# Performance work log

Measured on AMD Instinct MI355X. Metric: run time of the kernel, lower is better.

The kernel has to match this reference:

```python
import jax, jax.numpy as jnp
import numpy as np

B, CN, CC, D, V = 65536, 16, 16, 128, 65
EPS = 1e-05

def setup_inputs() -> dict:
    key = jax.random.key(0)
    ks = jax.random.split(key, 7)
    x_num = jax.random.normal(ks[0], (B, CN), dtype=jnp.float32)
    x_cat = jax.random.randint(ks[1], (B, CC), 0, V, dtype=jnp.int32)
    means = jax.random.normal(ks[2], (CN,), dtype=jnp.float32)
    stds = jax.random.uniform(ks[3], (CN,), dtype=jnp.float32, minval=0.5, maxval=2.0)
    lin_W = jax.random.normal(ks[4], (CN, D), dtype=jnp.float32) * 0.02  # Linear(1,D) weight per numeric attr
    lin_b = jax.random.normal(ks[5], (CN, D), dtype=jnp.float32) * 0.02
    emb = jax.random.normal(ks[6], (CC, V, D), dtype=jnp.float32) * 0.02  # stacked embedding tables
    return {"x_num": x_num, "means": means, "stds": stds, "lin_W": lin_W,
            "lin_b": lin_b, "emb": emb, "x_cat": x_cat}

def reference(x_num, means, stds, lin_W, lin_b, emb, x_cat):
    # numeric attrs: sigmoid((x - mean)/(std + eps)) -> Linear(1,D), summed over attrs
    z = jax.nn.sigmoid((x_num - means) / (stds + EPS))          # [B, CN]
    h = jnp.einsum('bi,id->bd', z, lin_W) + lin_b.sum(axis=0)   # [B, D]
    # categorical attrs: per-attr embedding lookup, summed over attrs
    gathered = emb[jnp.arange(emb.shape[0]), x_cat]             # [B, CC, D]
    return h + gathered.sum(axis=1)                              # [B, D]
```

## Files before the change

kernel.cpp:

```cpp
#include <hip/hip_runtime.h>


constexpr int CN = 16;
constexpr int CC = 16;
constexpr int D  = 128;
constexpr int V  = 65;
constexpr float EPS = 1e-5f;

constexpr int W      = 16;
constexpr int NSLICE = D / W;
constexpr int RPB    = 512;
constexpr int TILE   = 64;
constexpr int NTILE  = RPB / TILE;
constexpr int PAD    = 20;

__device__ __forceinline__ unsigned short f2bf(float f) {
    unsigned u = __float_as_uint(f);
    u = (u + 0x7fffu + ((u >> 16) & 1u)) >> 16;
    return (unsigned short)u;
}

__device__ __forceinline__ void fma4(float s, const float4& w, float4& a) {
    a.x += s * w.x; a.y += s * w.y; a.z += s * w.z; a.w += s * w.w;
}

__device__ __forceinline__ void gacc(const unsigned short* p, float4& a) {
    const uint2 g = *(const uint2*)p;
    a.x += __uint_as_float(g.x << 16);
    a.y += __uint_as_float(g.x & 0xffff0000u);
    a.z += __uint_as_float(g.y << 16);
    a.w += __uint_as_float(g.y & 0xffff0000u);
}

__global__ __launch_bounds__(256, 3) void embed_att_kernel(
    const float* __restrict__ x_num,
    const float* __restrict__ means,
    const float* __restrict__ stds,
    const float* __restrict__ lin_W,
    const float* __restrict__ lin_b,
    const float* __restrict__ emb,
    const int*  __restrict__ x_cat,
    float* __restrict__ out)
{
    __shared__ unsigned short emb_s[CC * V * W];
    __shared__ float z_s[2][TILE][PAD];
    __shared__ int   idx_s[2][TILE][PAD];

    const int tid = threadIdx.x;
    const int l   = tid & 3;
    const int l4  = l * 4;
    const int rr  = tid >> 2;
    const int d0  = blockIdx.y * W;
    const int row_base = blockIdx.x * RPB;

    float4 wf[CN];
    float4 bs = make_float4(0.f, 0.f, 0.f, 0.f);
#pragma unroll
    for (int i = 0; i < CN; ++i) {
        wf[i] = *(const float4*)&lin_W[i * D + d0 + l4];
        const float4 b = *(const float4*)&lin_b[i * D + d0 + l4];
        bs.x += b.x; bs.y += b.y; bs.z += b.z; bs.w += b.w;
    }
    const float4 mm = *(const float4*)&means[l4];
    const float4 sv = *(const float4*)&stds[l4];
    const float LOG2E = 1.44269504088896340736f;
    float4 inv;
    inv.x = -LOG2E / (sv.x + EPS); inv.y = -LOG2E / (sv.y + EPS);
    inv.z = -LOG2E / (sv.z + EPS); inv.w = -LOG2E / (sv.w + EPS);

    for (int j = tid; j < CC * V * W / 4; j += 256) {
        const int seg = j >> 2, k = j & 3;
        const float4 e = *(const float4*)&emb[seg * D + d0 + k * 4];
        uint2 p;
        p.x = (unsigned)f2bf(e.x) | ((unsigned)f2bf(e.y) << 16);
        p.y = (unsigned)f2bf(e.z) | ((unsigned)f2bf(e.w) << 16);
        *(uint2*)&emb_s[seg * W + k * 4] = p;
    }

    float4 xf; int4 xi;
    {
        const int row = row_base + rr;
        xf = *(const float4*)&x_num[row * CN + l4];
        xi = *(const int4*)&x_cat[row * CC + l4];
    }

    for (int t = 0; t < NTILE; ++t) {
        const int buf = t & 1;
        float4 z;
        z.x = 1.f / (1.f + __builtin_amdgcn_exp2f((xf.x - mm.x) * inv.x));
        z.y = 1.f / (1.f + __builtin_amdgcn_exp2f((xf.y - mm.y) * inv.y));
        z.z = 1.f / (1.f + __builtin_amdgcn_exp2f((xf.z - mm.z) * inv.z));
        z.w = 1.f / (1.f + __builtin_amdgcn_exp2f((xf.w - mm.w) * inv.w));
        *(float4*)&z_s[buf][rr][l4] = z;
        *(int4*)&idx_s[buf][rr][l4] = xi;
        __syncthreads();

        if (t + 1 < NTILE) {
            const int row = row_base + (t + 1) * TILE + rr;
            xf = *(const float4*)&x_num[row * CN + l4];
            xi = *(const int4*)&x_cat[row * CC + l4];
        }

        const int4 i0 = *(const int4*)&idx_s[buf][rr][0];
        const int4 i1 = *(const int4*)&idx_s[buf][rr][4];
        const int4 i2 = *(const int4*)&idx_s[buf][rr][8];
        const int4 i3 = *(const int4*)&idx_s[buf][rr][12];
        const float4 z0 = *(const float4*)&z_s[buf][rr][0];
        const float4 z1 = *(const float4*)&z_s[buf][rr][4];
        const float4 z2 = *(const float4*)&z_s[buf][rr][8];
        const float4 z3 = *(const float4*)&z_s[buf][rr][12];

        float4 acc = bs;
        fma4(z0.x, wf[0],  acc); fma4(z0.y, wf[1],  acc);
        fma4(z0.z, wf[2],  acc); fma4(z0.w, wf[3],  acc);
        fma4(z1.x, wf[4],  acc); fma4(z1.y, wf[5],  acc);
        fma4(z1.z, wf[6],  acc); fma4(z1.w, wf[7],  acc);
        fma4(z2.x, wf[8],  acc); fma4(z2.y, wf[9],  acc);
        fma4(z2.z, wf[10], acc); fma4(z2.w, wf[11], acc);
        fma4(z3.x, wf[12], acc); fma4(z3.y, wf[13], acc);
        fma4(z3.z, wf[14], acc); fma4(z3.w, wf[15], acc);

#define GAT(c, ix) gacc(&emb_s[((c) * V + (ix)) * W + l4], acc)
        GAT(0,  i0.x); GAT(1,  i0.y); GAT(2,  i0.z); GAT(3,  i0.w);
        GAT(4,  i1.x); GAT(5,  i1.y); GAT(6,  i1.z); GAT(7,  i1.w);
        GAT(8,  i2.x); GAT(9,  i2.y); GAT(10, i2.z); GAT(11, i2.w);
        GAT(12, i3.x); GAT(13, i3.y); GAT(14, i3.z); GAT(15, i3.w);
#undef GAT

        const int row = row_base + t * TILE + rr;
        *(float4*)&out[row * D + d0 + l4] = acc;
    }
}

extern "C" void kernel_launch(void* const* d_in, const int* in_sizes, int n_in,
                              void* d_out, int out_size, void* d_ws, size_t ws_size,
                              hipStream_t stream) {
    const float* x_num = (const float*)d_in[0];
    const float* means = (const float*)d_in[1];
    const float* stds  = (const float*)d_in[2];
    const float* lin_W = (const float*)d_in[3];
    const float* lin_b = (const float*)d_in[4];
    const float* emb   = (const float*)d_in[5];
    const int*   x_cat = (const int*)d_in[6];
    float* out = (float*)d_out;

    const int B      = in_sizes[0] / CN;
    const int nchunk = B / RPB;

    dim3 grid(nchunk, NSLICE, 1);
    embed_att_kernel<<<grid, 256, 0, stream>>>(x_num, means, stds, lin_W, lin_b,
                                               emb, x_cat, out);
}
```

Measured before the change: 99.45 us.

## Make z/idx staging wave-private, drop per-tile barrier, pad embedding rows

Each wavefront now stages its own 16 rows of sigmoid values and indices in a private shared-memory slice, so the per-tile block-wide barrier is removed and only one barrier remains after the embedding table load. The bf16 embedding rows in LDS are padded from 16 to 20 elements to spread random gather accesses across banks. The aim is to cut barrier stalls and LDS bank conflicts. The cost is more LDS for the table (about 41.6 KB versus 33 KB), which may limit blocks per CU, and the code relies on the wavefront lockstep ordering of each wave's own write and subsequent read.

```diff
diff --git a/kernel.cpp b/kernel.cpp
--- a/kernel.cpp
+++ b/kernel.cpp
@@ -12,7 +12,8 @@
 constexpr int RPB    = 512;
 constexpr int TILE   = 64;
 constexpr int NTILE  = RPB / TILE;
-constexpr int PAD    = 20;
+constexpr int EPAD   = 20;
+constexpr int ZPAD   = 20;
 
 __device__ __forceinline__ unsigned short f2bf(float f) {
     unsigned u = __float_as_uint(f);
@@ -42,14 +43,16 @@
     const int*  __restrict__ x_cat,
     float* __restrict__ out)
 {
-    __shared__ unsigned short emb_s[CC * V * W];
-    __shared__ float z_s[2][TILE][PAD];
-    __shared__ int   idx_s[2][TILE][PAD];
+    __shared__ unsigned short emb_s[CC * V * EPAD];
+    __shared__ float z_s[4][16][ZPAD];
+    __shared__ int   idx_s[4][16][ZPAD];
 
     const int tid = threadIdx.x;
     const int l   = tid & 3;
     const int l4  = l * 4;
     const int rr  = tid >> 2;
+    const int w   = tid >> 6;
+    const int rw  = rr & 15;
     const int d0  = blockIdx.y * W;
     const int row_base = blockIdx.x * RPB;
 
@@ -68,13 +71,13 @@
     inv.x = -LOG2E / (sv.x + EPS); inv.y = -LOG2E / (sv.y + EPS);
     inv.z = -LOG2E / (sv.z + EPS); inv.w = -LOG2E / (sv.w + EPS);
 
-    for (int j = tid; j < CC * V * W / 4; j += 256) {
+    for (int j = tid; j < CC * V * 4; j += 256) {
         const int seg = j >> 2, k = j & 3;
         const float4 e = *(const float4*)&emb[seg * D + d0 + k * 4];
         uint2 p;
         p.x = (unsigned)f2bf(e.x) | ((unsigned)f2bf(e.y) << 16);
         p.y = (unsigned)f2bf(e.z) | ((unsigned)f2bf(e.w) << 16);
-        *(uint2*)&emb_s[seg * W + k * 4] = p;
+        *(uint2*)&emb_s[seg * EPAD + k * 4] = p;
     }
 
     float4 xf; int4 xi;
@@ -84,16 +87,16 @@
         xi = *(const int4*)&x_cat[row * CC + l4];
     }
 
+    __syncthreads();
+
     for (int t = 0; t < NTILE; ++t) {
-        const int buf = t & 1;
         float4 z;
         z.x = 1.f / (1.f + __builtin_amdgcn_exp2f((xf.x - mm.x) * inv.x));
         z.y = 1.f / (1.f + __builtin_amdgcn_exp2f((xf.y - mm.y) * inv.y));
         z.z = 1.f / (1.f + __builtin_amdgcn_exp2f((xf.z - mm.z) * inv.z));
         z.w = 1.f / (1.f + __builtin_amdgcn_exp2f((xf.w - mm.w) * inv.w));
-        *(float4*)&z_s[buf][rr][l4] = z;
-        *(int4*)&idx_s[buf][rr][l4] = xi;
-        __syncthreads();
+        *(float4*)&z_s[w][rw][l4] = z;
+        *(int4*)&idx_s[w][rw][l4] = xi;
 
         if (t + 1 < NTILE) {
             const int row = row_base + (t + 1) * TILE + rr;
@@ -101,14 +104,14 @@
             xi = *(const int4*)&x_cat[row * CC + l4];
         }
 
-        const int4 i0 = *(const int4*)&idx_s[buf][rr][0];
-        const int4 i1 = *(const int4*)&idx_s[buf][rr][4];
-        const int4 i2 = *(const int4*)&idx_s[buf][rr][8];
-        const int4 i3 = *(const int4*)&idx_s[buf][rr][12];
-        const float4 z0 = *(const float4*)&z_s[buf][rr][0];
-        const float4 z1 = *(const float4*)&z_s[buf][rr][4];
-        const float4 z2 = *(const float4*)&z_s[buf][rr][8];
-        const float4 z3 = *(const float4*)&z_s[buf][rr][12];
+        const int4 i0 = *(const int4*)&idx_s[w][rw][0];
+        const int4 i1 = *(const int4*)&idx_s[w][rw][4];
+        const int4 i2 = *(const int4*)&idx_s[w][rw][8];
+        const int4 i3 = *(const int4*)&idx_s[w][rw][12];
+        const float4 z0 = *(const float4*)&z_s[w][rw][0];
+        const float4 z1 = *(const float4*)&z_s[w][rw][4];
+        const float4 z2 = *(const float4*)&z_s[w][rw][8];
+        const float4 z3 = *(const float4*)&z_s[w][rw][12];
 
         float4 acc = bs;
         fma4(z0.x, wf[0],  acc); fma4(z0.y, wf[1],  acc);
@@ -120,7 +123,7 @@
         fma4(z3.x, wf[12], acc); fma4(z3.y, wf[13], acc);
         fma4(z3.z, wf[14], acc); fma4(z3.w, wf[15], acc);
 
-#define GAT(c, ix) gacc(&emb_s[((c) * V + (ix)) * W + l4], acc)
+#define GAT(c, ix) gacc(&emb_s[((c) * V + (ix)) * EPAD + l4], acc)
         GAT(0,  i0.x); GAT(1,  i0.y); GAT(2,  i0.z); GAT(3,  i0.w);
         GAT(4,  i1.x); GAT(5,  i1.y); GAT(6,  i1.z); GAT(7,  i1.w);
         GAT(8,  i2.x); GAT(9,  i2.y); GAT(10, i2.z); GAT(11, i2.w);
```

Result: no change. 100.8 us (+1.4%).
